# Performance work log

Hardware: AMD Instinct MI355X
Metric: run time of the kernel (lower is better)

Reference implementation:

```python
import jax, jax.numpy as jnp
import numpy as np

DIM = 1024
NUM_HEADS = 16
HEAD_D = DIM // NUM_HEADS


def setup_inputs() -> dict:
    key = jax.random.key(0)
    ks = jax.random.split(key, 9)
    B, T, D = 4, 2048, DIM
    s = 1.0 / np.sqrt(D)
    return {
        "x": jax.random.normal(ks[0], (B, T, D), dtype=jnp.float32),
        "Wq": jax.random.normal(ks[1], (D, D), dtype=jnp.float32) * s,
        "bq": jnp.zeros((D,), dtype=jnp.float32),
        "Wk": jax.random.normal(ks[2], (D, D), dtype=jnp.float32) * s,
        "bk": jnp.zeros((D,), dtype=jnp.float32),
        "Wv": jax.random.normal(ks[3], (D, D), dtype=jnp.float32) * s,
        "bv": jnp.zeros((D,), dtype=jnp.float32),
        "Wo": jax.random.normal(ks[4], (D, D), dtype=jnp.float32) * s,
        "bo": jnp.zeros((D,), dtype=jnp.float32),
    }


def reference(x, Wq, bq, Wk, bk, Wv, bv, Wo, bo):
    B, T, D = x.shape
    H, Hd = NUM_HEADS, HEAD_D
    # QKV projections (torch Linear: x @ W.T + b)
    q = (x @ Wq.T + bq).reshape(B, T, H, Hd).transpose(0, 2, 1, 3)  # [B,H,T,Hd]
    k = (x @ Wk.T + bk).reshape(B, T, H, Hd).transpose(0, 2, 1, 3)
    v = (x @ Wv.T + bv).reshape(B, T, H, Hd).transpose(0, 2, 1, 3)
    scores = jnp.einsum("bhqd,bhkd->bhqk", q, k) / jnp.sqrt(jnp.float32(Hd))
    probs = jax.nn.softmax(scores, axis=-1)
    out = jnp.einsum("bhqk,bhkd->bhqd", probs, v)  # [B,H,T,Hd]
    out = out.transpose(0, 2, 1, 3).reshape(B, T, D)
    return out @ Wo.T + bo
```

## Files before the change

### kernel.cpp

```cpp
#include <hip/hip_runtime.h>

typedef unsigned short u16;
typedef unsigned int   u32;
typedef __bf16 bf16;
typedef __attribute__((ext_vector_type(8))) __bf16 bf16x8;
typedef __attribute__((ext_vector_type(4))) float  f32x4;


__device__ __forceinline__ u16 f2bf(float f) {
  u32 u = __float_as_uint(f);
  u32 r = (u + 0x7fffu + ((u >> 16) & 1u)) >> 16;
  return (u16)r;
}

__device__ __forceinline__ void gload_lds16(const void* g, void* l) {
  __builtin_amdgcn_global_load_lds((__attribute__((address_space(1))) u32*)g,
                                   (__attribute__((address_space(3))) u32*)l,
                                   16, 0, 0);
}

__device__ __forceinline__ u32 cvt_pk_bf16(float lo, float hi) {
  u32 r;
  asm("v_cvt_pk_bf16_f32 %0, %1, %2" : "=v"(r) : "v"(lo), "v"(hi));
  return r;
}


__global__ __launch_bounds__(256) void cvt_bf16_kernel(const float* __restrict__ in,
                                                       u16* __restrict__ out, int n4) {
  int i = blockIdx.x * blockDim.x + threadIdx.x;
  int stride = gridDim.x * blockDim.x;
  for (; i < n4; i += stride) {
    float4 v = ((const float4*)in)[i];
    uint2 o;
    o.x = (u32)f2bf(v.x) | ((u32)f2bf(v.y) << 16);
    o.y = (u32)f2bf(v.z) | ((u32)f2bf(v.w) << 16);
    ((uint2*)out)[i] = o;
  }
}


#define GM 8192
#define GN 1024
#define GK 1024

template <int MODE>
__global__ __launch_bounds__(256) void gemm_bt_kernel(const u16* __restrict__ A,
                                                      const u16* __restrict__ W,
                                                      const float* __restrict__ bias,
                                                      void* __restrict__ Cout) {
  __shared__ u16 sA[2][128 * 32];
  __shared__ u16 sB[2][128 * 32];

  const int tid  = threadIdx.x;
  const int lane = tid & 63;
  const int w    = tid >> 6;
  const int wm   = w >> 1, wn = w & 1;
  const int lid  = (blockIdx.x & 7) * 64 + (blockIdx.x >> 3);
  const int tn   = lid & 7;
  const int tm   = lid >> 3;
  const int m0   = tm * 128, n0 = tn * 128;
  const int rgrp = lane >> 4, rlo = lane & 15;

  auto stage = [&](int buf, int kt) {
    int k0 = kt * 32;
    #pragma unroll
    for (int r = 0; r < 2; ++r) {
      int c   = (w * 2 + r) * 64 + lane;
      int row = c >> 2;
      int cb  = c & 3;
      int col = ((cb ^ (row & 3)) * 8);
      gload_lds16(A + (size_t)(m0 + row) * GK + k0 + col, &sA[buf][(w * 2 + r) * 512]);
      gload_lds16(W + (size_t)(n0 + row) * GK + k0 + col, &sB[buf][(w * 2 + r) * 512]);
    }
  };

  f32x4 acc[4][4] = {};

  stage(0, 0);
  asm volatile("s_waitcnt vmcnt(0)" ::: "memory");
  __syncthreads();

  for (int kt = 0; kt < GK / 32; ++kt) {
    int buf = kt & 1;
    if (kt + 1 < GK / 32) stage(buf ^ 1, kt + 1);

    bf16x8 a[4], b[4];
    #pragma unroll
    for (int i = 0; i < 4; ++i) {
      int row = wm * 64 + i * 16 + rlo;
      int cb  = rgrp ^ (row & 3);
      a[i] = *(const bf16x8*)&sA[buf][row * 32 + cb * 8];
    }
    #pragma unroll
    for (int j = 0; j < 4; ++j) {
      int row = wn * 64 + j * 16 + rlo;
      int cb  = rgrp ^ (row & 3);
      b[j] = *(const bf16x8*)&sB[buf][row * 32 + cb * 8];
    }
    #pragma unroll
    for (int i = 0; i < 4; ++i)
      #pragma unroll
      for (int j = 0; j < 4; ++j)
        acc[i][j] = __builtin_amdgcn_mfma_f32_16x16x32_bf16(a[i], b[j], acc[i][j], 0, 0, 0);

    asm volatile("s_waitcnt vmcnt(0)" ::: "memory");
    __syncthreads();
  }

  #pragma unroll
  for (int i = 0; i < 4; ++i) {
    #pragma unroll
    for (int j = 0; j < 4; ++j) {
      #pragma unroll
      for (int r = 0; r < 4; ++r) {
        int m = m0 + wm * 64 + i * 16 + rgrp * 4 + r;
        int n = n0 + wn * 64 + j * 16 + rlo;
        float v = acc[i][j][r] + bias[n];
        if (MODE == 0) {
          int b = m >> 11, t = m & 2047, h = n >> 6, hd = n & 63;
          ((bf16*)Cout)[(((size_t)(b * 16 + h) * 2048 + t) << 6) + hd] = (bf16)v;
        } else if (MODE == 1) {
          int b = m >> 11, t = m & 2047, h = n >> 6, hd = n & 63;
          ((bf16*)Cout)[((size_t)(b * 16 + h) * 64 + hd) * 2048 + t] = (bf16)v;
        } else {
          ((float*)Cout)[(size_t)m * GN + n] = v;
        }
      }
    }
  }
}


__global__ __launch_bounds__(256) void attn_kernel(const u16* __restrict__ Q,
                                                   const u16* __restrict__ K,
                                                   const u16* __restrict__ Vt,
                                                   bf16* __restrict__ O) {
  __shared__ u16 sK[2][64 * 64];
  __shared__ u16 sV[2][64 * 64];

  const int tid  = threadIdx.x;
  const int lane = tid & 63;
  const int w    = tid >> 6;
  const int rgrp = lane >> 4, rlo = lane & 15;
  const int bid  = (blockIdx.x & 7) * 256 + (blockIdx.x >> 3);
  const int qt   = bid & 31;
  const int bh   = bid >> 5;
  const float SCL = 0.125f * 1.44269504089f;

  const u16* Qh = Q  + (size_t)bh * 2048 * 64;
  const u16* Kh = K  + (size_t)bh * 2048 * 64;
  const u16* Vh = Vt + (size_t)bh * 64 * 2048;

  auto stage = [&](int buf, int t) {
    #pragma unroll
    for (int r = 0; r < 2; ++r) {
      int c   = (w * 2 + r) * 64 + lane;
      int row = c >> 3;
      int cb  = c & 7;
      int col = (cb ^ (row & 7)) * 8;
      gload_lds16(Kh + ((size_t)(t * 64 + row)) * 64 + col, &sK[buf][(w * 2 + r) * 512]);
      gload_lds16(Vh + (size_t)row * 2048 + t * 64 + col,   &sV[buf][(w * 2 + r) * 512]);
    }
  };

  stage(0, 0);

  bf16x8 bQ[2];
  {
    int q0 = qt * 64 + w * 16 + rlo;
    bQ[0] = *(const bf16x8*)&Qh[(size_t)q0 * 64 + rgrp * 8];
    bQ[1] = *(const bf16x8*)&Qh[(size_t)q0 * 64 + 32 + rgrp * 8];
  }

  asm volatile("s_waitcnt vmcnt(0)" ::: "memory");
  __syncthreads();

  float lsum = 0.f;
  f32x4 o[4] = {};

  for (int t = 0; t < 32; ++t) {
    const int cur = t & 1;
    if (t + 1 < 32) stage(cur ^ 1, t + 1);

    f32x4 sT[4];
    #pragma unroll
    for (int nt = 0; nt < 4; ++nt) {
      sT[nt] = (f32x4){0.f, 0.f, 0.f, 0.f};
      #pragma unroll
      for (int kk = 0; kk < 2; ++kk) {
        int row = nt * 16 + rlo;
        int cb  = (kk * 4 + rgrp) ^ (row & 7);
        bf16x8 aK = *(const bf16x8*)&sK[cur][row * 64 + cb * 8];
        sT[nt] = __builtin_amdgcn_mfma_f32_16x16x32_bf16(aK, bQ[kk], sT[nt], 0, 0, 0);
      }
    }

    #pragma unroll
    for (int nt = 0; nt < 4; ++nt)
      #pragma unroll
      for (int r = 0; r < 4; ++r)
        sT[nt][r] = __builtin_amdgcn_exp2f(sT[nt][r] * SCL);
    #pragma unroll
    for (int nt = 0; nt < 4; ++nt)
      lsum += (sT[nt][0] + sT[nt][1]) + (sT[nt][2] + sT[nt][3]);

    u32 pw[4][2];
    #pragma unroll
    for (int nt = 0; nt < 4; ++nt) {
      pw[nt][0] = cvt_pk_bf16(sT[nt][0], sT[nt][1]);
      pw[nt][1] = cvt_pk_bf16(sT[nt][2], sT[nt][3]);
    }

    bf16x8 bP[2];
    #pragma unroll
    for (int kk = 0; kk < 2; ++kk) {
      u32 a0 = pw[2 * kk][0], b0 = pw[2 * kk + 1][0];
      u32 a1 = pw[2 * kk][1], b1 = pw[2 * kk + 1][1];
      asm("v_permlane32_swap_b32 %0, %1" : "+v"(a0), "+v"(b0));
      asm("v_permlane16_swap_b32 %0, %1" : "+v"(a0), "+v"(b0));
      asm("v_permlane32_swap_b32 %0, %1" : "+v"(a1), "+v"(b1));
      asm("v_permlane16_swap_b32 %0, %1" : "+v"(a1), "+v"(b1));
      union { u32 u[4]; bf16x8 v; } fu;
      fu.u[0] = a0; fu.u[1] = a1; fu.u[2] = b0; fu.u[3] = b1;
      bP[kk] = fu.v;
    }

    #pragma unroll
    for (int kk = 0; kk < 2; ++kk)
      #pragma unroll
      for (int dt = 0; dt < 4; ++dt) {
        int rowv = dt * 16 + rlo;
        int cbv  = (kk * 4 + rgrp) ^ (rowv & 7);
        bf16x8 aV = *(const bf16x8*)&sV[cur][rowv * 64 + cbv * 8];
        o[dt] = __builtin_amdgcn_mfma_f32_16x16x32_bf16(aV, bP[kk], o[dt], 0, 0, 0);
      }

    asm volatile("s_waitcnt vmcnt(0)" ::: "memory");
    __syncthreads();
  }

  lsum += __shfl_xor(lsum, 16);
  lsum += __shfl_xor(lsum, 32);
  const float inv = 1.0f / lsum;

  const int b = bh >> 4, h = bh & 15;
  const int tq = qt * 64 + w * 16 + rlo;
  #pragma unroll
  for (int dt = 0; dt < 4; ++dt) {
    uint2 st;
    st.x = cvt_pk_bf16(o[dt][0] * inv, o[dt][1] * inv);
    st.y = cvt_pk_bf16(o[dt][2] * inv, o[dt][3] * inv);
    *(uint2*)&O[((size_t)(b * 2048 + tq)) * 1024 + h * 64 + dt * 16 + rgrp * 4] = st;
  }
}


extern "C" void kernel_launch(void* const* d_in, const int* in_sizes, int n_in,
                              void* d_out, int out_size, void* d_ws, size_t ws_size,
                              hipStream_t stream) {
  const float* x  = (const float*)d_in[0];
  const float* Wq = (const float*)d_in[1];
  const float* bq = (const float*)d_in[2];
  const float* Wk = (const float*)d_in[3];
  const float* bk = (const float*)d_in[4];
  const float* Wv = (const float*)d_in[5];
  const float* bv = (const float*)d_in[6];
  const float* Wo = (const float*)d_in[7];
  const float* bo = (const float*)d_in[8];

  char* ws = (char*)d_ws;
  u16* xb  = (u16*)(ws);
  u16* Wqb = (u16*)(ws + 16777216);
  u16* Wkb = (u16*)(ws + 18874368);
  u16* Wvb = (u16*)(ws + 20971520);
  u16* Wob = (u16*)(ws + 23068672);
  u16* Qb  = (u16*)(ws + 25165824);
  u16* Kb  = (u16*)(ws + 41943040);
  u16* Vtb = (u16*)(ws + 58720256);
  u16* Ab  = (u16*)(ws + 75497472);

  cvt_bf16_kernel<<<4096, 256, 0, stream>>>(x,  xb,  8388608 / 4);
  cvt_bf16_kernel<<<1024, 256, 0, stream>>>(Wq, Wqb, 1048576 / 4);
  cvt_bf16_kernel<<<1024, 256, 0, stream>>>(Wk, Wkb, 1048576 / 4);
  cvt_bf16_kernel<<<1024, 256, 0, stream>>>(Wv, Wvb, 1048576 / 4);
  cvt_bf16_kernel<<<1024, 256, 0, stream>>>(Wo, Wob, 1048576 / 4);

  gemm_bt_kernel<0><<<512, 256, 0, stream>>>(xb, Wqb, bq, Qb);
  gemm_bt_kernel<0><<<512, 256, 0, stream>>>(xb, Wkb, bk, Kb);
  gemm_bt_kernel<1><<<512, 256, 0, stream>>>(xb, Wvb, bv, Vtb);

  attn_kernel<<<2048, 256, 0, stream>>>(Qb, Kb, Vtb, (bf16*)Ab);

  gemm_bt_kernel<2><<<512, 256, 0, stream>>>(Ab, Wob, bo, d_out);
}
```

Measured before the change: 251.7 us.

## Batch QKV GEMMs and weight casts, double queries per attention wave

Merges the four weight conversions into one launch and the three QKV projection GEMMs into one 1536-block launch, which cuts launch count and tail effects. The softmax scale is folded into K at projection time, which removes a multiply per score. Each attention wave now handles two 16-query groups that share every K/V LDS fragment, which halves K/V traffic per query, and s_setprio is raised around the MFMA sections. In exchange there are more registers per wave and half as many attention blocks, and rounding K after scaling changes numerics slightly.

```diff
diff --git a/kernel.cpp b/kernel.cpp
--- a/kernel.cpp
+++ b/kernel.cpp
@@ -24,6 +24,8 @@
   asm("v_cvt_pk_bf16_f32 %0, %1, %2" : "=v"(r) : "v"(lo), "v"(hi));
   return r;
 }
+
+#define SCL_LOG2E 0.1803368801111204f
 
 
 __global__ __launch_bounds__(256) void cvt_bf16_kernel(const float* __restrict__ in,
@@ -39,16 +41,129 @@
   }
 }
 
-
-#define GM 8192
+__global__ __launch_bounds__(256) void cvt4_kernel(const float* __restrict__ p0,
+                                                   const float* __restrict__ p1,
+                                                   const float* __restrict__ p2,
+                                                   const float* __restrict__ p3,
+                                                   u16* o0, u16* o1, u16* o2, u16* o3) {
+  const int which = blockIdx.x >> 8;
+  const float* in = which == 0 ? p0 : which == 1 ? p1 : which == 2 ? p2 : p3;
+  u16* out = which == 0 ? o0 : which == 1 ? o1 : which == 2 ? o2 : o3;
+  int i = (blockIdx.x & 255) * 256 + threadIdx.x;
+  #pragma unroll
+  for (int r = 0; r < 4; ++r, i += 65536) {
+    float4 v = ((const float4*)in)[i];
+    uint2 o;
+    o.x = (u32)f2bf(v.x) | ((u32)f2bf(v.y) << 16);
+    o.y = (u32)f2bf(v.z) | ((u32)f2bf(v.w) << 16);
+    ((uint2*)out)[i] = o;
+  }
+}
+
+
+#define GK 1024
 #define GN 1024
-#define GK 1024
-
-template <int MODE>
-__global__ __launch_bounds__(256) void gemm_bt_kernel(const u16* __restrict__ A,
-                                                      const u16* __restrict__ W,
-                                                      const float* __restrict__ bias,
-                                                      void* __restrict__ Cout) {
+
+__global__ __launch_bounds__(256) void gemm_qkv_kernel(const u16* __restrict__ A,
+                                                       const u16* __restrict__ Wq,
+                                                       const u16* __restrict__ Wk,
+                                                       const u16* __restrict__ Wv,
+                                                       const float* __restrict__ bq,
+                                                       const float* __restrict__ bk,
+                                                       const float* __restrict__ bv,
+                                                       u16* __restrict__ Qo,
+                                                       u16* __restrict__ Ko,
+                                                       u16* __restrict__ Vo) {
+  __shared__ u16 sA[2][128 * 32];
+  __shared__ u16 sB[2][128 * 32];
+
+  const int tid  = threadIdx.x;
+  const int lane = tid & 63;
+  const int w    = tid >> 6;
+  const int wm   = w >> 1, wn = w & 1;
+  const int lid  = (blockIdx.x & 7) * 192 + (blockIdx.x >> 3);
+  const int which = lid >> 9;
+  const int sub   = lid & 511;
+  const u16*  W    = which == 0 ? Wq : which == 1 ? Wk : Wv;
+  const float* bias = which == 0 ? bq : which == 1 ? bk : bv;
+  const int tn   = sub & 7;
+  const int tm   = sub >> 3;
+  const int m0   = tm * 128, n0 = tn * 128;
+  const int rgrp = lane >> 4, rlo = lane & 15;
+
+  auto stage = [&](int buf, int kt) {
+    int k0 = kt * 32;
+    #pragma unroll
+    for (int r = 0; r < 2; ++r) {
+      int c   = (w * 2 + r) * 64 + lane;
+      int row = c >> 2;
+      int cb  = c & 3;
+      int col = ((cb ^ (row & 3)) * 8);
+      gload_lds16(A + (size_t)(m0 + row) * GK + k0 + col, &sA[buf][(w * 2 + r) * 512]);
+      gload_lds16(W + (size_t)(n0 + row) * GK + k0 + col, &sB[buf][(w * 2 + r) * 512]);
+    }
+  };
+
+  f32x4 acc[4][4] = {};
+
+  stage(0, 0);
+  asm volatile("s_waitcnt vmcnt(0)" ::: "memory");
+  __syncthreads();
+
+  for (int kt = 0; kt < GK / 32; ++kt) {
+    int buf = kt & 1;
+    if (kt + 1 < GK / 32) stage(buf ^ 1, kt + 1);
+
+    bf16x8 a[4], b[4];
+    #pragma unroll
+    for (int i = 0; i < 4; ++i) {
+      int row = wm * 64 + i * 16 + rlo;
+      int cb  = rgrp ^ (row & 3);
+      a[i] = *(const bf16x8*)&sA[buf][row * 32 + cb * 8];
+    }
+    #pragma unroll
+    for (int j = 0; j < 4; ++j) {
+      int row = wn * 64 + j * 16 + rlo;
+      int cb  = rgrp ^ (row & 3);
+      b[j] = *(const bf16x8*)&sB[buf][row * 32 + cb * 8];
+    }
+    #pragma unroll
+    for (int i = 0; i < 4; ++i)
+      #pragma unroll
+      for (int j = 0; j < 4; ++j)
+        acc[i][j] = __builtin_amdgcn_mfma_f32_16x16x32_bf16(a[i], b[j], acc[i][j], 0, 0, 0);
+
+    asm volatile("s_waitcnt vmcnt(0)" ::: "memory");
+    __syncthreads();
+  }
+
+  #pragma unroll
+  for (int i = 0; i < 4; ++i) {
+    #pragma unroll
+    for (int j = 0; j < 4; ++j) {
+      #pragma unroll
+      for (int r = 0; r < 4; ++r) {
+        int m = m0 + wm * 64 + i * 16 + rgrp * 4 + r;
+        int n = n0 + wn * 64 + j * 16 + rlo;
+        float v = acc[i][j][r] + bias[n];
+        int b = m >> 11, t = m & 2047, h = n >> 6, hd = n & 63;
+        if (which == 0) {
+          Qo[(((size_t)(b * 16 + h) * 2048 + t) << 6) + hd] = (u16)__builtin_bit_cast(u16, (bf16)v);
+        } else if (which == 1) {
+          Ko[(((size_t)(b * 16 + h) * 2048 + t) << 6) + hd] =
+              (u16)__builtin_bit_cast(u16, (bf16)(v * SCL_LOG2E));
+        } else {
+          Vo[((size_t)(b * 16 + h) * 64 + hd) * 2048 + t] = (u16)__builtin_bit_cast(u16, (bf16)v);
+        }
+      }
+    }
+  }
+}
+
+__global__ __launch_bounds__(256) void gemm_out_kernel(const u16* __restrict__ A,
+                                                       const u16* __restrict__ W,
+                                                       const float* __restrict__ bias,
+                                                       float* __restrict__ Cout) {
   __shared__ u16 sA[2][128 * 32];
   __shared__ u16 sB[2][128 * 32];
 
@@ -109,26 +224,15 @@
   }
 
   #pragma unroll
-  for (int i = 0; i < 4; ++i) {
-    #pragma unroll
-    for (int j = 0; j < 4; ++j) {
+  for (int i = 0; i < 4; ++i)
+    #pragma unroll
+    for (int j = 0; j < 4; ++j)
       #pragma unroll
       for (int r = 0; r < 4; ++r) {
         int m = m0 + wm * 64 + i * 16 + rgrp * 4 + r;
         int n = n0 + wn * 64 + j * 16 + rlo;
-        float v = acc[i][j][r] + bias[n];
-        if (MODE == 0) {
-          int b = m >> 11, t = m & 2047, h = n >> 6, hd = n & 63;
-          ((bf16*)Cout)[(((size_t)(b * 16 + h) * 2048 + t) << 6) + hd] = (bf16)v;
-        } else if (MODE == 1) {
-          int b = m >> 11, t = m & 2047, h = n >> 6, hd = n & 63;
-          ((bf16*)Cout)[((size_t)(b * 16 + h) * 64 + hd) * 2048 + t] = (bf16)v;
-        } else {
-          ((float*)Cout)[(size_t)m * GN + n] = v;
-        }
-      }
-    }
-  }
+        Cout[(size_t)m * GN + n] = acc[i][j][r] + bias[n];
+      }
 }
 
 
@@ -143,10 +247,9 @@
   const int lane = tid & 63;
   const int w    = tid >> 6;
   const int rgrp = lane >> 4, rlo = lane & 15;
-  const int bid  = (blockIdx.x & 7) * 256 + (blockIdx.x >> 3);
-  const int qt   = bid & 31;
-  const int bh   = bid >> 5;
-  const float SCL = 0.125f * 1.44269504089f;
+  const int bid  = (blockIdx.x & 7) * 128 + (blockIdx.x >> 3);
+  const int qt   = bid & 15;
+  const int bh   = bid >> 4;
 
   const u16* Qh = Q  + (size_t)bh * 2048 * 64;
   const u16* Kh = K  + (size_t)bh * 2048 * 64;
@@ -166,66 +269,79 @@
 
   stage(0, 0);
 
-  bf16x8 bQ[2];
-  {
-    int q0 = qt * 64 + w * 16 + rlo;
-    bQ[0] = *(const bf16x8*)&Qh[(size_t)q0 * 64 + rgrp * 8];
-    bQ[1] = *(const bf16x8*)&Qh[(size_t)q0 * 64 + 32 + rgrp * 8];
+  bf16x8 bQ[2][2];
+  #pragma unroll
+  for (int qg = 0; qg < 2; ++qg) {
+    int q0 = qt * 128 + w * 32 + qg * 16 + rlo;
+    bQ[qg][0] = *(const bf16x8*)&Qh[(size_t)q0 * 64 + rgrp * 8];
+    bQ[qg][1] = *(const bf16x8*)&Qh[(size_t)q0 * 64 + 32 + rgrp * 8];
   }
 
   asm volatile("s_waitcnt vmcnt(0)" ::: "memory");
   __syncthreads();
 
-  float lsum = 0.f;
-  f32x4 o[4] = {};
+  float lsum[2] = {0.f, 0.f};
+  f32x4 o[2][4] = {};
 
   for (int t = 0; t < 32; ++t) {
     const int cur = t & 1;
     if (t + 1 < 32) stage(cur ^ 1, t + 1);
 
-    f32x4 sT[4];
+    f32x4 sT[2][4];
     #pragma unroll
     for (int nt = 0; nt < 4; ++nt) {
-      sT[nt] = (f32x4){0.f, 0.f, 0.f, 0.f};
+      sT[0][nt] = (f32x4){0.f, 0.f, 0.f, 0.f};
+      sT[1][nt] = (f32x4){0.f, 0.f, 0.f, 0.f};
+    }
+    __builtin_amdgcn_s_setprio(1);
+    #pragma unroll
+    for (int nt = 0; nt < 4; ++nt)
       #pragma unroll
       for (int kk = 0; kk < 2; ++kk) {
         int row = nt * 16 + rlo;
         int cb  = (kk * 4 + rgrp) ^ (row & 7);
         bf16x8 aK = *(const bf16x8*)&sK[cur][row * 64 + cb * 8];
-        sT[nt] = __builtin_amdgcn_mfma_f32_16x16x32_bf16(aK, bQ[kk], sT[nt], 0, 0, 0);
-      }
-    }
-
-    #pragma unroll
-    for (int nt = 0; nt < 4; ++nt)
-      #pragma unroll
-      for (int r = 0; r < 4; ++r)
-        sT[nt][r] = __builtin_amdgcn_exp2f(sT[nt][r] * SCL);
-    #pragma unroll
-    for (int nt = 0; nt < 4; ++nt)
-      lsum += (sT[nt][0] + sT[nt][1]) + (sT[nt][2] + sT[nt][3]);
-
-    u32 pw[4][2];
-    #pragma unroll
-    for (int nt = 0; nt < 4; ++nt) {
-      pw[nt][0] = cvt_pk_bf16(sT[nt][0], sT[nt][1]);
-      pw[nt][1] = cvt_pk_bf16(sT[nt][2], sT[nt][3]);
-    }
-
-    bf16x8 bP[2];
-    #pragma unroll
-    for (int kk = 0; kk < 2; ++kk) {
-      u32 a0 = pw[2 * kk][0], b0 = pw[2 * kk + 1][0];
-      u32 a1 = pw[2 * kk][1], b1 = pw[2 * kk + 1][1];
-      asm("v_permlane32_swap_b32 %0, %1" : "+v"(a0), "+v"(b0));
-      asm("v_permlane16_swap_b32 %0, %1" : "+v"(a0), "+v"(b0));
-      asm("v_permlane32_swap_b32 %0, %1" : "+v"(a1), "+v"(b1));
-      asm("v_permlane16_swap_b32 %0, %1" : "+v"(a1), "+v"(b1));
-      union { u32 u[4]; bf16x8 v; } fu;
-      fu.u[0] = a0; fu.u[1] = a1; fu.u[2] = b0; fu.u[3] = b1;
-      bP[kk] = fu.v;
-    }
-
+        sT[0][nt] = __builtin_amdgcn_mfma_f32_16x16x32_bf16(aK, bQ[0][kk], sT[0][nt], 0, 0, 0);
+        sT[1][nt] = __builtin_amdgcn_mfma_f32_16x16x32_bf16(aK, bQ[1][kk], sT[1][nt], 0, 0, 0);
+      }
+    __builtin_amdgcn_s_setprio(0);
+
+    #pragma unroll
+    for (int qg = 0; qg < 2; ++qg) {
+      #pragma unroll
+      for (int nt = 0; nt < 4; ++nt)
+        #pragma unroll
+        for (int r = 0; r < 4; ++r)
+          sT[qg][nt][r] = __builtin_amdgcn_exp2f(sT[qg][nt][r]);
+      #pragma unroll
+      for (int nt = 0; nt < 4; ++nt)
+        lsum[qg] += (sT[qg][nt][0] + sT[qg][nt][1]) + (sT[qg][nt][2] + sT[qg][nt][3]);
+    }
+
+    bf16x8 bP[2][2];
+    #pragma unroll
+    for (int qg = 0; qg < 2; ++qg) {
+      u32 pw[4][2];
+      #pragma unroll
+      for (int nt = 0; nt < 4; ++nt) {
+        pw[nt][0] = cvt_pk_bf16(sT[qg][nt][0], sT[qg][nt][1]);
+        pw[nt][1] = cvt_pk_bf16(sT[qg][nt][2], sT[qg][nt][3]);
+      }
+      #pragma unroll
+      for (int kk = 0; kk < 2; ++kk) {
+        u32 a0 = pw[2 * kk][0], b0 = pw[2 * kk + 1][0];
+        u32 a1 = pw[2 * kk][1], b1 = pw[2 * kk + 1][1];
+        asm("v_permlane32_swap_b32 %0, %1" : "+v"(a0), "+v"(b0));
+        asm("v_permlane16_swap_b32 %0, %1" : "+v"(a0), "+v"(b0));
+        asm("v_permlane32_swap_b32 %0, %1" : "+v"(a1), "+v"(b1));
+        asm("v_permlane16_swap_b32 %0, %1" : "+v"(a1), "+v"(b1));
+        union { u32 u[4]; bf16x8 v; } fu;
+        fu.u[0] = a0; fu.u[1] = a1; fu.u[2] = b0; fu.u[3] = b1;
+        bP[qg][kk] = fu.v;
+      }
+    }
+
+    __builtin_amdgcn_s_setprio(1);
     #pragma unroll
     for (int kk = 0; kk < 2; ++kk)
       #pragma unroll
@@ -233,25 +349,30 @@
         int rowv = dt * 16 + rlo;
         int cbv  = (kk * 4 + rgrp) ^ (rowv & 7);
         bf16x8 aV = *(const bf16x8*)&sV[cur][rowv * 64 + cbv * 8];
-        o[dt] = __builtin_amdgcn_mfma_f32_16x16x32_bf16(aV, bP[kk], o[dt], 0, 0, 0);
-      }
+        o[0][dt] = __builtin_amdgcn_mfma_f32_16x16x32_bf16(aV, bP[0][kk], o[0][dt], 0, 0, 0);
+        o[1][dt] = __builtin_amdgcn_mfma_f32_16x16x32_bf16(aV, bP[1][kk], o[1][dt], 0, 0, 0);
+      }
+    __builtin_amdgcn_s_setprio(0);
 
     asm volatile("s_waitcnt vmcnt(0)" ::: "memory");
     __syncthreads();
   }
 
-  lsum += __shfl_xor(lsum, 16);
-  lsum += __shfl_xor(lsum, 32);
-  const float inv = 1.0f / lsum;
-
   const int b = bh >> 4, h = bh & 15;
-  const int tq = qt * 64 + w * 16 + rlo;
   #pragma unroll
-  for (int dt = 0; dt < 4; ++dt) {
-    uint2 st;
-    st.x = cvt_pk_bf16(o[dt][0] * inv, o[dt][1] * inv);
-    st.y = cvt_pk_bf16(o[dt][2] * inv, o[dt][3] * inv);
-    *(uint2*)&O[((size_t)(b * 2048 + tq)) * 1024 + h * 64 + dt * 16 + rgrp * 4] = st;
+  for (int qg = 0; qg < 2; ++qg) {
+    float ls = lsum[qg];
+    ls += __shfl_xor(ls, 16);
+    ls += __shfl_xor(ls, 32);
+    const float inv = 1.0f / ls;
+    const int tq = qt * 128 + w * 32 + qg * 16 + rlo;
+    #pragma unroll
+    for (int dt = 0; dt < 4; ++dt) {
+      uint2 st;
+      st.x = cvt_pk_bf16(o[qg][dt][0] * inv, o[qg][dt][1] * inv);
+      st.y = cvt_pk_bf16(o[qg][dt][2] * inv, o[qg][dt][3] * inv);
+      *(uint2*)&O[((size_t)(b * 2048 + tq)) * 1024 + h * 64 + dt * 16 + rgrp * 4] = st;
+    }
   }
 }
 
@@ -280,17 +401,12 @@
   u16* Vtb = (u16*)(ws + 58720256);
   u16* Ab  = (u16*)(ws + 75497472);
 
-  cvt_bf16_kernel<<<4096, 256, 0, stream>>>(x,  xb,  8388608 / 4);
-  cvt_bf16_kernel<<<1024, 256, 0, stream>>>(Wq, Wqb, 1048576 / 4);
-  cvt_bf16_kernel<<<1024, 256, 0, stream>>>(Wk, Wkb, 1048576 / 4);
-  cvt_bf16_kernel<<<1024, 256, 0, stream>>>(Wv, Wvb, 1048576 / 4);
-  cvt_bf16_kernel<<<1024, 256, 0, stream>>>(Wo, Wob, 1048576 / 4);
-
-  gemm_bt_kernel<0><<<512, 256, 0, stream>>>(xb, Wqb, bq, Qb);
-  gemm_bt_kernel<0><<<512, 256, 0, stream>>>(xb, Wkb, bk, Kb);
-  gemm_bt_kernel<1><<<512, 256, 0, stream>>>(xb, Wvb, bv, Vtb);
-
-  attn_kernel<<<2048, 256, 0, stream>>>(Qb, Kb, Vtb, (bf16*)Ab);
-
-  gemm_bt_kernel<2><<<512, 256, 0, stream>>>(Ab, Wob, bo, d_out);
-}
+  cvt_bf16_kernel<<<4096, 256, 0, stream>>>(x, xb, 8388608 / 4);
+  cvt4_kernel<<<1024, 256, 0, stream>>>(Wq, Wk, Wv, Wo, Wqb, Wkb, Wvb, Wob);
+
+  gemm_qkv_kernel<<<1536, 256, 0, stream>>>(xb, Wqb, Wkb, Wvb, bq, bk, bv, Qb, Kb, Vtb);
+
+  attn_kernel<<<1024, 256, 0, stream>>>(Qb, Kb, Vtb, (bf16*)Ab);
+
+  gemm_out_kernel<<<512, 256, 0, stream>>>(Ab, Wob, bo, (float*)d_out);
+}
```

Result: no change. 253.2 us (+0.6%).
